# Kernel tuning notes

Hardware: AMD Instinct MI355X
Metric: run time of the kernel (lower is better)

The kernel has to match this reference:

```python
import jax, jax.numpy as jnp
import numpy as np

L_SEQ, BS = 500, 512
STATE, OBS, INP = 64, 64, 32  # estimate_A = eye(obs) acts on state -> state == obs


def setup_inputs() -> dict:
    key = jax.random.key(0)
    ks = jax.random.split(key, 8)
    return {
        "external_input_seq": jax.random.normal(ks[0], (L_SEQ, BS, INP), jnp.float32),
        "observations_seq": jax.random.normal(ks[1], (L_SEQ, BS, OBS), jnp.float32),
        "initial_prior_mu": jax.random.normal(ks[2], (BS, STATE), jnp.float32),
        # sigma must be strictly positive (log is taken); shift uniform away from 0
        "initial_prior_sigma": jax.random.uniform(ks[3], (BS, STATE), jnp.float32) + 0.5,
        # learned params (torch randn init, scaled 0.1 for numerical stability of the recursion)
        "logsigma": jax.random.normal(ks[4], (STATE,), jnp.float32) * 0.1,
        "B": jax.random.normal(ks[5], (STATE, INP), jnp.float32) * 0.1,
        "H": jax.random.normal(ks[6], (OBS, STATE), jnp.float32) * 0.1,
        "logdelta": jax.random.normal(ks[7], (OBS,), jnp.float32) * 0.1,
    }


def reference(external_input_seq, observations_seq, initial_prior_mu,
              initial_prior_sigma, logsigma, B, H, logdelta):
    s = initial_prior_mu.shape[-1]
    dt = initial_prior_mu.dtype
    A = jnp.eye(s, dtype=dt)                    # estimate_A = eye, requires_grad=False
    I = jnp.eye(s, dtype=dt)
    Q = jnp.diag(jnp.exp(logsigma) ** 2)        # process noise cov (s, s)
    Rm = jnp.diag(jnp.exp(logdelta) ** 2)       # observation noise cov (o, o)

    def step(carry, inp):
        mu_prior, cov_prior = carry             # (bs, s), (bs, s, s)
        u_prev, y = inp                         # (bs, inp), (bs, o)
        mu_pred = mu_prior @ A.T + u_prev @ B.T                     # (bs, s)
        cov_pred = A @ cov_prior @ A.T + Q                          # (bs, s, s)
        S = H @ cov_pred @ H.T + Rm                                 # (bs, o, o)
        K = cov_pred @ H.T @ jnp.linalg.inv(S)                      # (bs, s, o)
        innov = y - mu_pred @ H.T                                   # (bs, o)
        mu_post = mu_pred + jnp.einsum('bso,bo->bs', K, innov)      # (bs, s)
        cov_post = (I - K @ H) @ cov_pred                           # (bs, s, s)
        logsig = jnp.log(jnp.sqrt(jnp.diagonal(cov_post, axis1=-2, axis2=-1)))
        return (mu_post, cov_post), (mu_post, logsig)

    cov0 = (initial_prior_sigma ** 2)[..., None] * jnp.eye(s, dtype=dt)  # diag_embed
    _, (mus, logs) = jax.lax.scan(
        step, (initial_prior_mu, cov0),
        (external_input_seq[:-1], observations_seq[1:]))
    state_mu = jnp.concatenate([initial_prior_mu[None], mus], axis=0)          # (l, bs, s)
    state_logsigma = jnp.concatenate([jnp.log(initial_prior_sigma)[None], logs], axis=0)
    return state_mu, state_logsigma
```

## Files before the change

kernel.cpp:

```cpp
#include <hip/hip_runtime.h>
#include <math.h>

#define L_SEQ 500
#define NBS   512
#define N     64
#define NI    32
#define AUGW  132
#define PW    68
#define HW    68

#define OFF_AUG 0
#define OFF_P   (OFF_AUG + 64*AUGW)
#define OFF_H   (OFF_P   + 64*PW)
#define OFF_BT  (OFF_H   + 64*HW)
#define OFF_RK  (OFF_BT  + NI*64)
#define OFF_QD  (OFF_RK  + 64)
#define OFF_RD  (OFF_QD  + 64)
#define OFF_MU  (OFF_RD  + 64)
#define OFF_MUP (OFF_MU  + 64)
#define OFF_WV  (OFF_MUP + 64)
#define OFF_U   (OFF_WV  + 64)
#define OFF_YV  (OFF_U   + 32)
#define OFF_LSC (OFF_YV  + 64)
#define OFF_FLG (OFF_LSC + 64)
#define SM_FLOATS (OFF_FLG + 4)

#define CONV_TAU  2e-5f
#define CONV_MINS 20

union F4 { float4 v; float f[4]; };

#define LW(i,k) Aug[((i)-16)*AUGW + 48 + (k)]

__global__ __launch_bounds__(256, 2)
void akf5(const float* __restrict__ ext,
          const float* __restrict__ obs,
          const float* __restrict__ mu0,
          const float* __restrict__ sg0,
          const float* __restrict__ lsg,
          const float* __restrict__ Bm,
          const float* __restrict__ Hm,
          const float* __restrict__ ldl,
          float* __restrict__ out_mu,
          float* __restrict__ out_ls)
{
    extern __shared__ float sm[];
    float* Aug = sm + OFF_AUG;
    float* P   = sm + OFF_P;
    float* Hs  = sm + OFF_H;
    float* Bt  = sm + OFF_BT;
    float* rk  = sm + OFF_RK;
    float* Qd  = sm + OFF_QD;
    float* Rd  = sm + OFF_RD;
    float* mu  = sm + OFF_MU;
    float* mup = sm + OFF_MUP;
    float* wv  = sm + OFF_WV;
    float* uvec= sm + OFF_U;
    float* yv  = sm + OFF_YV;
    float* lsc = sm + OFF_LSC;
    int*   flagI = (int*)(sm + OFF_FLG);

    const int b   = blockIdx.x;
    const int tid = threadIdx.x;
    const int tx  = tid & 15;
    const int ty  = tid >> 4;

    int Rlow = 0, Clow = 0;
    {
        int t = tid < 136 ? tid : 0;
        int R = (int)((sqrtf(8.0f * (float)t + 1.0f) - 1.0f) * 0.5f);
        if ((R + 1) * (R + 2) / 2 <= t) ++R;
        if (R * (R + 1) / 2 > t) --R;
        Rlow = R; Clow = t - R * (R + 1) / 2;
    }

    if (tid < 64) {
        int i = tid;
        float q = expf(lsg[i]); Qd[i] = q * q;
        float r = expf(ldl[i]); Rd[i] = r * r;
        float m0 = mu0[b * N + i];
        float s0 = sg0[b * N + i];
        mu[i]  = m0;
        mup[i] = s0;
        out_mu[(size_t)b * N + i] = m0;
        out_ls[(size_t)b * N + i] = logf(s0);
        Aug[i * AUGW + 129] = 0.f; Aug[i * AUGW + 130] = 0.f; Aug[i * AUGW + 131] = 0.f;
    }
    if (tid == 0) { flagI[0] = 0; flagI[1] = 0; }
    for (int e = tid; e < N * N; e += 256) {
        Hs[(e >> 6) * HW + (e & 63)] = Hm[e];
    }
    for (int e = tid; e < N * NI; e += 256) {
        int i = e >> 5, k = e & 31;
        Bt[k * 64 + i] = Bm[e];
    }
    __syncthreads();
    for (int e = tid; e < N * N; e += 256) {
        int i = e >> 6, j = e & 63;
        float v = 0.f;
        if (i == j) { float s = mup[i]; v = s * s; }
        P[i * PW + j] = v;
    }
    if (tid >= 192 && tid < 200) {
        int q = tid - 192;
        *(float4*)&uvec[4 * q] = *(const float4*)&ext[(size_t)b * NI + 4 * q];
    }
    if (tid >= 200 && tid < 216) {
        int q = tid - 200;
        *(float4*)&yv[4 * q] = *(const float4*)&obs[(size_t)(NBS + b) * N + 4 * q];
    }
    __syncthreads();

    int streak = 0, sb = 0;

    #pragma unroll 1
    for (int s = 0; s < L_SEQ - 1; ++s) {
        if (tid < 64) {
            float acc = mu[tid];
            #pragma unroll
            for (int k = 0; k < NI; ++k) acc += Bt[k * 64 + tid] * uvec[k];
            mup[tid] = acc;
        }
        __builtin_amdgcn_wave_barrier();
        if (tid < 64) {
            float acc = yv[tid];
            #pragma unroll 4
            for (int c4 = 0; c4 < 16; ++c4) {
                F4 h; h.v = *(const float4*)&Hs[tid * HW + 4 * c4];
                F4 m; m.v = *(const float4*)&mup[4 * c4];
                acc -= h.f[0]*m.f[0] + h.f[1]*m.f[1] + h.f[2]*m.f[2] + h.f[3]*m.f[3];
            }
            Aug[tid * AUGW + 128] = acc;
        }
        {
            const int i0 = 4 * ty, j0 = 4 * tx;
            float acc[4][4];
            F4 qv; qv.v = *(const float4*)&Qd[j0];
            #pragma unroll
            for (int dr = 0; dr < 4; ++dr) {
                F4 hv; hv.v = *(const float4*)&Hs[(i0 + dr) * HW + j0];
                #pragma unroll
                for (int dc = 0; dc < 4; ++dc) acc[dr][dc] = hv.f[dc] * qv.f[dc];
            }
            #pragma unroll 4
            for (int c4 = 0; c4 < 16; ++c4) {
                F4 h4[4], p4[4];
                #pragma unroll
                for (int dr = 0; dr < 4; ++dr) h4[dr].v = *(const float4*)&Hs[(i0 + dr) * HW + 4 * c4];
                #pragma unroll
                for (int dk = 0; dk < 4; ++dk) p4[dk].v = *(const float4*)&P[(4 * c4 + dk) * PW + j0];
                #pragma unroll
                for (int dk = 0; dk < 4; ++dk)
                    #pragma unroll
                    for (int dr = 0; dr < 4; ++dr)
                        #pragma unroll
                        for (int dc = 0; dc < 4; ++dc)
                            acc[dr][dc] += h4[dr].f[dk] * p4[dk].f[dc];
            }
            #pragma unroll
            for (int dr = 0; dr < 4; ++dr) {
                float4 v; v.x = acc[dr][0]; v.y = acc[dr][1]; v.z = acc[dr][2]; v.w = acc[dr][3];
                *(float4*)&Aug[(i0 + dr) * AUGW + 64 + j0] = v;
            }
        }
        __syncthreads();

        if (tid < 136) {
            const int i0 = 4 * Rlow, j0 = 4 * Clow;
            float acc[4][4];
            #pragma unroll
            for (int a = 0; a < 4; ++a)
                #pragma unroll
                for (int c = 0; c < 4; ++c) acc[a][c] = 0.f;
            #pragma unroll 4
            for (int c4 = 0; c4 < 16; ++c4) {
                F4 a4[4], b4[4];
                #pragma unroll
                for (int dr = 0; dr < 4; ++dr) a4[dr].v = *(const float4*)&Aug[(i0 + dr) * AUGW + 64 + 4 * c4];
                #pragma unroll
                for (int dc = 0; dc < 4; ++dc) b4[dc].v = *(const float4*)&Hs[(j0 + dc) * HW + 4 * c4];
                #pragma unroll
                for (int dr = 0; dr < 4; ++dr)
                    #pragma unroll
                    for (int dc = 0; dc < 4; ++dc)
                        #pragma unroll
                        for (int dk = 0; dk < 4; ++dk)
                            acc[dr][dc] += a4[dr].f[dk] * b4[dc].f[dk];
            }
            #pragma unroll
            for (int dr = 0; dr < 4; ++dr) {
                #pragma unroll
                for (int dc = 0; dc < 4; ++dc)
                    if (i0 + dr == j0 + dc) acc[dr][dc] += Rd[i0 + dr];
                float4 v; v.x = acc[dr][0]; v.y = acc[dr][1]; v.z = acc[dr][2]; v.w = acc[dr][3];
                *(float4*)&Aug[(i0 + dr) * AUGW + j0] = v;
            }
        } else if (tid < 200) {
            const int i = tid - 136;
            P[i * PW + i] += Qd[i];
        } else if (tid == 200) {
            flagI[0] = 0; flagI[1] = 0;
        }
        __syncthreads();

        #pragma unroll 1
        for (int p = 0; p < 4; ++p) {
            const int p0 = 16 * p;
            if (tid < 64) {
                const int lane = tid;
                float st[16], lw[16], myrk = 0.f;
                if (lane >= p0) {
                    #pragma unroll
                    for (int q = 0; q < 4; ++q) {
                        F4 t4; t4.v = *(const float4*)&Aug[lane * AUGW + p0 + 4 * q];
                        st[4*q+0] = t4.f[0]; st[4*q+1] = t4.f[1]; st[4*q+2] = t4.f[2]; st[4*q+3] = t4.f[3];
                    }
                } else {
                    #pragma unroll
                    for (int q = 0; q < 16; ++q) st[q] = 0.f;
                }
                #pragma unroll
                for (int kr = 0; kr < 16; ++kr) {
                    const int k = p0 + kr;
                    float dk  = __shfl(st[kr], k, 64);
                    float rkv = 1.0f / dk;
                    if (lane == k) myrk = rkv;
                    float coef = st[kr] * rkv;
                    coef = (lane > k) ? coef : 0.f;
                    lw[kr] = coef;
                    #pragma unroll
                    for (int jr = kr + 1; jr < 16; ++jr) {
                        float wjk = __shfl(st[kr], p0 + jr, 64);
                        st[jr] -= coef * wjk;
                    }
                }
                if (lane >= p0) {
                    #pragma unroll
                    for (int q = 0; q < 4; ++q) {
                        float4 v; v.x = st[4*q+0]; v.y = st[4*q+1]; v.z = st[4*q+2]; v.w = st[4*q+3];
                        *(float4*)&Aug[lane * AUGW + p0 + 4 * q] = v;
                    }
                    if (lane < p0 + 16) rk[lane] = myrk;
                }
                if (lane >= p0 + 16) {
                    #pragma unroll
                    for (int q = 0; q < 4; ++q) {
                        float4 v; v.x = lw[4*q+0]; v.y = lw[4*q+1]; v.z = lw[4*q+2]; v.w = lw[4*q+3];
                        *(float4*)&LW(lane, 4 * q) = v;
                    }
                }
                float ec[16], zr[16];
                #pragma unroll
                for (int r2 = 0; r2 < 16; ++r2) {
                    ec[r2] = Aug[(p0 + r2) * AUGW + 64 + lane];
                    zr[r2] = Aug[(p0 + r2) * AUGW + 128];
                }
                #pragma unroll
                for (int kp = 0; kp < 15; ++kp) {
                    #pragma unroll
                    for (int r2 = kp + 1; r2 < 16; ++r2) {
                        float L = __shfl(lw[kp], p0 + r2, 64);
                        ec[r2] -= L * ec[kp];
                        zr[r2] -= L * zr[kp];
                    }
                }
                #pragma unroll
                for (int r2 = 0; r2 < 16; ++r2)
                    Aug[(p0 + r2) * AUGW + 64 + lane] = ec[r2];
                if (lane == 0) {
                    #pragma unroll
                    for (int r2 = 0; r2 < 16; ++r2)
                        Aug[(p0 + r2) * AUGW + 128] = zr[r2];
                }
            }
            __syncthreads();

            if (p < 3) {
                const int TS  = (p == 0) ? 78 : (p == 1) ? 36 : 10;
                const int rows = 48 - 16 * p;
                const int TE  = (rows / 4) * 17;
                const int tot = TS + TE;
                const int ofs = 4 * (p + 1);
                #pragma unroll 1
                for (int t = tid; t < tot; t += 256) {
                    int i0, Cb; bool isS;
                    if (t < TS) {
                        int rr = (int)((sqrtf(8.0f * (float)t + 1.0f) - 1.0f) * 0.5f);
                        if ((rr + 1) * (rr + 2) / 2 <= t) ++rr;
                        if (rr * (rr + 1) / 2 > t) --rr;
                        int cc = t - rr * (rr + 1) / 2;
                        i0 = 4 * (ofs + rr); Cb = 4 * (ofs + cc); isS = true;
                    } else {
                        int e2 = t - TS;
                        i0 = 4 * (ofs + e2 / 17); Cb = 64 + 4 * (e2 % 17); isS = false;
                    }
                    F4 acc[4];
                    #pragma unroll
                    for (int dr = 0; dr < 4; ++dr) acc[dr].v = *(const float4*)&Aug[(i0 + dr) * AUGW + Cb];
                    #pragma unroll
                    for (int c4 = 0; c4 < 4; ++c4) {
                        F4 a4[4];
                        #pragma unroll
                        for (int dr = 0; dr < 4; ++dr) a4[dr].v = *(const float4*)&LW(i0 + dr, 4 * c4);
                        if (isS) {
                            F4 b4[4];
                            #pragma unroll
                            for (int dc = 0; dc < 4; ++dc) b4[dc].v = *(const float4*)&Aug[(Cb + dc) * AUGW + p0 + 4 * c4];
                            #pragma unroll
                            for (int dr = 0; dr < 4; ++dr)
                                #pragma unroll
                                for (int dc = 0; dc < 4; ++dc)
                                    #pragma unroll
                                    for (int dk = 0; dk < 4; ++dk)
                                        acc[dr].f[dc] -= a4[dr].f[dk] * b4[dc].f[dk];
                        } else {
                            F4 b4[4];
                            #pragma unroll
                            for (int dk = 0; dk < 4; ++dk) b4[dk].v = *(const float4*)&Aug[(p0 + 4 * c4 + dk) * AUGW + Cb];
                            #pragma unroll
                            for (int dk = 0; dk < 4; ++dk)
                                #pragma unroll
                                for (int dr = 0; dr < 4; ++dr)
                                    #pragma unroll
                                    for (int dc = 0; dc < 4; ++dc)
                                        acc[dr].f[dc] -= a4[dr].f[dk] * b4[dk].f[dc];
                        }
                    }
                    #pragma unroll
                    for (int dr = 0; dr < 4; ++dr) *(float4*)&Aug[(i0 + dr) * AUGW + Cb] = acc[dr].v;
                }
                __syncthreads();
            }
        }

        const size_t o = (size_t)((s + 1) * NBS + b) * N;
        float tdmax = 0.f, tpmax = 0.f;
        if (tid < 136) {
            const int i0 = 4 * Rlow, j0 = 4 * Clow;
            F4 acc[4], oldv[4];
            #pragma unroll
            for (int dr = 0; dr < 4; ++dr) { acc[dr].v = *(const float4*)&P[(i0 + dr) * PW + j0]; oldv[dr].v = acc[dr].v; }
            #pragma unroll 2
            for (int c4 = 0; c4 < 16; ++c4) {
                F4 rv; rv.v = *(const float4*)&rk[4 * c4];
                F4 ea[4], eb[4];
                #pragma unroll
                for (int dk = 0; dk < 4; ++dk) ea[dk].v = *(const float4*)&Aug[(4 * c4 + dk) * AUGW + 64 + i0];
                #pragma unroll
                for (int dk = 0; dk < 4; ++dk) eb[dk].v = *(const float4*)&Aug[(4 * c4 + dk) * AUGW + 64 + j0];
                #pragma unroll
                for (int dk = 0; dk < 4; ++dk) {
                    float sc[4];
                    #pragma unroll
                    for (int dr = 0; dr < 4; ++dr) sc[dr] = ea[dk].f[dr] * rv.f[dk];
                    #pragma unroll
                    for (int dr = 0; dr < 4; ++dr)
                        #pragma unroll
                        for (int dc = 0; dc < 4; ++dc)
                            acc[dr].f[dc] -= sc[dr] * eb[dk].f[dc];
                }
            }
            #pragma unroll
            for (int dr = 0; dr < 4; ++dr) *(float4*)&P[(i0 + dr) * PW + j0] = acc[dr].v;
            #pragma unroll
            for (int dr = 0; dr < 4; ++dr)
                #pragma unroll
                for (int dc = 0; dc < 4; ++dc) {
                    float d = acc[dr].f[dc] - oldv[dr].f[dc];
                    if (Rlow == Clow && dr == dc) d += Qd[i0 + dr];
                    tdmax = fmaxf(tdmax, fabsf(d));
                    tpmax = fmaxf(tpmax, fabsf(acc[dr].f[dc]));
                }
            if (Rlow != Clow) {
                #pragma unroll
                for (int dc = 0; dc < 4; ++dc) {
                    float4 v; v.x = acc[0].f[dc]; v.y = acc[1].f[dc]; v.z = acc[2].f[dc]; v.w = acc[3].f[dc];
                    *(float4*)&P[(j0 + dc) * PW + i0] = v;
                }
            } else {
                #pragma unroll
                for (int dr = 0; dr < 4; ++dr)
                    out_ls[o + i0 + dr] = 0.5f * logf(acc[dr].f[dr]);
            }
        }
        if (tid >= 192) {
            const int i = tid - 192;
            wv[i] = rk[i] * Aug[i * AUGW + 128];
            float acc = mup[i];
            #pragma unroll 4
            for (int c4 = 0; c4 < 16; ++c4) {
                F4 wq; wq.v = *(const float4*)&wv[4 * c4];
                #pragma unroll
                for (int dk = 0; dk < 4; ++dk)
                    acc += Aug[(4 * c4 + dk) * AUGW + 64 + i] * wq.f[dk];
            }
            mu[i] = acc;
            out_mu[o + i] = acc;
        }
        if (tid >= 136 && tid < 144) {
            int q = tid - 136;
            *(float4*)&uvec[4 * q] = *(const float4*)&ext[(size_t)((s + 1) * NBS + b) * NI + 4 * q];
        }
        if (tid >= 144 && tid < 160 && s < L_SEQ - 2) {
            int q = tid - 144;
            *(float4*)&yv[4 * q] = *(const float4*)&obs[(size_t)((s + 2) * NBS + b) * N + 4 * q];
        }
        #pragma unroll
        for (int off = 32; off; off >>= 1) {
            tdmax = fmaxf(tdmax, __shfl_xor(tdmax, off, 64));
            tpmax = fmaxf(tpmax, __shfl_xor(tpmax, off, 64));
        }
        if ((tid & 63) == 0) {
            atomicMax(&flagI[0], __float_as_int(tdmax));
            atomicMax(&flagI[1], __float_as_int(tpmax));
        }
        __syncthreads();

        {
            float dm = __int_as_float(flagI[0]);
            float pm = __int_as_float(flagI[1]);
            bool conv = (s >= CONV_MINS) && (dm <= CONV_TAU * pm);
            streak = conv ? (streak + 1) : 0;
            if (streak >= 2) { sb = s + 1; break; }
        }
    }

    if (sb > 0) {
        {
            const int i0 = 4 * ty, j0 = 4 * tx;
            float acc[4][4];
            #pragma unroll
            for (int a = 0; a < 4; ++a)
                #pragma unroll
                for (int c = 0; c < 4; ++c) acc[a][c] = 0.f;
            #pragma unroll 4
            for (int c4 = 0; c4 < 16; ++c4) {
                F4 a4[4], b4[4];
                #pragma unroll
                for (int dr = 0; dr < 4; ++dr) a4[dr].v = *(const float4*)&P[(i0 + dr) * PW + 4 * c4];
                #pragma unroll
                for (int dc = 0; dc < 4; ++dc) b4[dc].v = *(const float4*)&Hs[(j0 + dc) * HW + 4 * c4];
                #pragma unroll
                for (int dr = 0; dr < 4; ++dr)
                    #pragma unroll
                    for (int dc = 0; dc < 4; ++dc)
                        #pragma unroll
                        for (int dk = 0; dk < 4; ++dk)
                            acc[dr][dc] += a4[dr].f[dk] * b4[dc].f[dk];
            }
            float ri[4];
            #pragma unroll
            for (int dc = 0; dc < 4; ++dc) ri[dc] = 1.0f / Rd[j0 + dc];
            #pragma unroll
            for (int dr = 0; dr < 4; ++dr) {
                float4 v; v.x = acc[dr][0]*ri[0]; v.y = acc[dr][1]*ri[1];
                          v.z = acc[dr][2]*ri[2]; v.w = acc[dr][3]*ri[3];
                *(float4*)&Aug[(i0 + dr) * AUGW + 64 + j0] = v;
            }
            if (tid < 64) lsc[tid] = 0.5f * logf(P[tid * PW + tid]);
        }
        __syncthreads();

        #pragma unroll 1
        for (int s2 = sb; s2 < L_SEQ - 1; ++s2) {
            const size_t o2 = (size_t)((s2 + 1) * NBS + b) * N;
            if (tid < 64) {
                float acc = mu[tid];
                #pragma unroll
                for (int k = 0; k < NI; ++k) acc += Bt[k * 64 + tid] * uvec[k];
                mup[tid] = acc;
            }
            __syncthreads();
            if (tid < 64) {
                float acc = yv[tid];
                #pragma unroll 4
                for (int c4 = 0; c4 < 16; ++c4) {
                    F4 h; h.v = *(const float4*)&Hs[tid * HW + 4 * c4];
                    F4 m; m.v = *(const float4*)&mup[4 * c4];
                    acc -= h.f[0]*m.f[0] + h.f[1]*m.f[1] + h.f[2]*m.f[2] + h.f[3]*m.f[3];
                }
                wv[tid] = acc;
                out_ls[o2 + tid] = lsc[tid];
            } else if (tid < 72) {
                int q = tid - 64;
                *(float4*)&uvec[4 * q] = *(const float4*)&ext[(size_t)((s2 + 1) * NBS + b) * NI + 4 * q];
            }
            __syncthreads();
            if (tid < 64) {
                float acc = mup[tid];
                #pragma unroll 4
                for (int c4 = 0; c4 < 16; ++c4) {
                    F4 kg; kg.v = *(const float4*)&Aug[tid * AUGW + 64 + 4 * c4];
                    F4 w;  w.v  = *(const float4*)&wv[4 * c4];
                    acc += kg.f[0]*w.f[0] + kg.f[1]*w.f[1] + kg.f[2]*w.f[2] + kg.f[3]*w.f[3];
                }
                mu[tid] = acc;
                out_mu[o2 + tid] = acc;
            } else if (tid < 80 && s2 < L_SEQ - 2) {
                int q = tid - 64;
                *(float4*)&yv[4 * q] = *(const float4*)&obs[(size_t)((s2 + 2) * NBS + b) * N + 4 * q];
            }
            __syncthreads();
        }
    }
}

extern "C" void kernel_launch(void* const* d_in, const int* in_sizes, int n_in,
                              void* d_out, int out_size, void* d_ws, size_t ws_size,
                              hipStream_t stream) {
    const float* ext = (const float*)d_in[0];
    const float* obs = (const float*)d_in[1];
    const float* mu0 = (const float*)d_in[2];
    const float* sg0 = (const float*)d_in[3];
    const float* lsg = (const float*)d_in[4];
    const float* Bm  = (const float*)d_in[5];
    const float* Hm  = (const float*)d_in[6];
    const float* ldl = (const float*)d_in[7];
    float* out_mu = (float*)d_out;
    float* out_ls = out_mu + (size_t)L_SEQ * NBS * N;

    size_t smem = (size_t)SM_FLOATS * sizeof(float);
    hipFuncSetAttribute(reinterpret_cast<const void*>(akf5),
                        hipFuncAttributeMaxDynamicSharedMemorySize, (int)smem);

    akf5<<<dim3(NBS), dim3(256), smem, stream>>>(
        ext, obs, mu0, sg0, lsg, Bm, Hm, ldl, out_mu, out_ls);
}
```

Before: 14.88 ms.

## Overlap covariance downdate with block LDL factorization and use readlane broadcasts

Moves the rank-update of the covariance into the per-panel loop so warps 1-3 accumulate each finished panel's contribution while warp 0 factorizes the next panel, leaving only the last panel for after the loop. Replaces cross-lane shuffles with readlane scalar broadcasts and the exact reciprocal with the hardware approximate reciprocal. The aim is to shorten the serial critical path per timestep, at the cost of extra registers held across panels and slightly lower reciprocal precision.

```diff
diff --git a/kernel.cpp b/kernel.cpp
--- a/kernel.cpp
+++ b/kernel.cpp
@@ -32,8 +32,12 @@
 
 #define LW(i,k) Aug[((i)-16)*AUGW + 48 + (k)]
 
+__device__ __forceinline__ float rl(float x, int srclane) {
+    return __int_as_float(__builtin_amdgcn_readlane(__float_as_int(x), srclane));
+}
+
 __global__ __launch_bounds__(256, 2)
-void akf5(const float* __restrict__ ext,
+void akf7(const float* __restrict__ ext,
           const float* __restrict__ obs,
           const float* __restrict__ mu0,
           const float* __restrict__ sg0,
@@ -73,6 +77,14 @@
         if (R * (R + 1) / 2 > t) --R;
         Rlow = R; Clow = t - R * (R + 1) / 2;
     }
+    int Rg = 0, Cg = 0;
+    {
+        int t = (tid >= 64 && tid < 200) ? (tid - 64) : 0;
+        int R = (int)((sqrtf(8.0f * (float)t + 1.0f) - 1.0f) * 0.5f);
+        if ((R + 1) * (R + 2) / 2 <= t) ++R;
+        if (R * (R + 1) / 2 > t) --R;
+        Rg = R; Cg = t - R * (R + 1) / 2;
+    }
 
     if (tid < 64) {
         int i = tid;
@@ -203,6 +215,7 @@
         }
         __syncthreads();
 
+        F4 gacc[4];
         #pragma unroll 1
         for (int p = 0; p < 4; ++p) {
             const int p0 = 16 * p;
@@ -222,15 +235,15 @@
                 #pragma unroll
                 for (int kr = 0; kr < 16; ++kr) {
                     const int k = p0 + kr;
-                    float dk  = __shfl(st[kr], k, 64);
-                    float rkv = 1.0f / dk;
+                    float dk  = rl(st[kr], k);
+                    float rkv = __builtin_amdgcn_rcpf(dk);
                     if (lane == k) myrk = rkv;
                     float coef = st[kr] * rkv;
                     coef = (lane > k) ? coef : 0.f;
                     lw[kr] = coef;
                     #pragma unroll
                     for (int jr = kr + 1; jr < 16; ++jr) {
-                        float wjk = __shfl(st[kr], p0 + jr, 64);
+                        float wjk = rl(st[kr], p0 + jr);
                         st[jr] -= coef * wjk;
                     }
                 }
@@ -259,7 +272,7 @@
                 for (int kp = 0; kp < 15; ++kp) {
                     #pragma unroll
                     for (int r2 = kp + 1; r2 < 16; ++r2) {
-                        float L = __shfl(lw[kp], p0 + r2, 64);
+                        float L = rl(lw[kp], p0 + r2);
                         ec[r2] -= L * ec[kp];
                         zr[r2] -= L * zr[kp];
                     }
@@ -271,6 +284,34 @@
                     #pragma unroll
                     for (int r2 = 0; r2 < 16; ++r2)
                         Aug[(p0 + r2) * AUGW + 128] = zr[r2];
+                }
+            } else if (p > 0 && tid < 200) {
+                const int cp = p - 1;
+                const int i0 = 4 * Rg, j0 = 4 * Cg;
+                if (p == 1) {
+                    #pragma unroll
+                    for (int dr = 0; dr < 4; ++dr) gacc[dr].v = *(const float4*)&P[(i0 + dr) * PW + j0];
+                }
+                #pragma unroll
+                for (int q = 0; q < 4; ++q) {
+                    const int c4 = 4 * cp + q;
+                    F4 rv; rv.v = *(const float4*)&rk[4 * c4];
+                    F4 ea[4], eb[4];
+                    #pragma unroll
+                    for (int dk = 0; dk < 4; ++dk) ea[dk].v = *(const float4*)&Aug[(4 * c4 + dk) * AUGW + 64 + i0];
+                    #pragma unroll
+                    for (int dk = 0; dk < 4; ++dk) eb[dk].v = *(const float4*)&Aug[(4 * c4 + dk) * AUGW + 64 + j0];
+                    #pragma unroll
+                    for (int dk = 0; dk < 4; ++dk) {
+                        float sc[4];
+                        #pragma unroll
+                        for (int dr = 0; dr < 4; ++dr) sc[dr] = ea[dk].f[dr] * rv.f[dk];
+                        #pragma unroll
+                        for (int dr = 0; dr < 4; ++dr)
+                            #pragma unroll
+                            for (int dc = 0; dc < 4; ++dc)
+                                gacc[dr].f[dc] -= sc[dr] * eb[dk].f[dc];
+                    }
                 }
             }
             __syncthreads();
@@ -335,13 +376,11 @@
 
         const size_t o = (size_t)((s + 1) * NBS + b) * N;
         float tdmax = 0.f, tpmax = 0.f;
-        if (tid < 136) {
-            const int i0 = 4 * Rlow, j0 = 4 * Clow;
-            F4 acc[4], oldv[4];
-            #pragma unroll
-            for (int dr = 0; dr < 4; ++dr) { acc[dr].v = *(const float4*)&P[(i0 + dr) * PW + j0]; oldv[dr].v = acc[dr].v; }
-            #pragma unroll 2
-            for (int c4 = 0; c4 < 16; ++c4) {
+        if (tid >= 64 && tid < 200) {
+            const int i0 = 4 * Rg, j0 = 4 * Cg;
+            #pragma unroll
+            for (int q = 0; q < 4; ++q) {
+                const int c4 = 12 + q;
                 F4 rv; rv.v = *(const float4*)&rk[4 * c4];
                 F4 ea[4], eb[4];
                 #pragma unroll
@@ -357,34 +396,35 @@
                     for (int dr = 0; dr < 4; ++dr)
                         #pragma unroll
                         for (int dc = 0; dc < 4; ++dc)
-                            acc[dr].f[dc] -= sc[dr] * eb[dk].f[dc];
-                }
-            }
-            #pragma unroll
-            for (int dr = 0; dr < 4; ++dr) *(float4*)&P[(i0 + dr) * PW + j0] = acc[dr].v;
-            #pragma unroll
-            for (int dr = 0; dr < 4; ++dr)
+                            gacc[dr].f[dc] -= sc[dr] * eb[dk].f[dc];
+                }
+            }
+            #pragma unroll
+            for (int dr = 0; dr < 4; ++dr) {
+                F4 oldv; oldv.v = *(const float4*)&P[(i0 + dr) * PW + j0];
                 #pragma unroll
                 for (int dc = 0; dc < 4; ++dc) {
-                    float d = acc[dr].f[dc] - oldv[dr].f[dc];
-                    if (Rlow == Clow && dr == dc) d += Qd[i0 + dr];
+                    float d = gacc[dr].f[dc] - oldv.f[dc];
+                    if (Rg == Cg && dr == dc) d += Qd[i0 + dr];
                     tdmax = fmaxf(tdmax, fabsf(d));
-                    tpmax = fmaxf(tpmax, fabsf(acc[dr].f[dc]));
-                }
-            if (Rlow != Clow) {
+                    tpmax = fmaxf(tpmax, fabsf(gacc[dr].f[dc]));
+                }
+            }
+            #pragma unroll
+            for (int dr = 0; dr < 4; ++dr) *(float4*)&P[(i0 + dr) * PW + j0] = gacc[dr].v;
+            if (Rg != Cg) {
                 #pragma unroll
                 for (int dc = 0; dc < 4; ++dc) {
-                    float4 v; v.x = acc[0].f[dc]; v.y = acc[1].f[dc]; v.z = acc[2].f[dc]; v.w = acc[3].f[dc];
+                    float4 v; v.x = gacc[0].f[dc]; v.y = gacc[1].f[dc]; v.z = gacc[2].f[dc]; v.w = gacc[3].f[dc];
                     *(float4*)&P[(j0 + dc) * PW + i0] = v;
                 }
             } else {
                 #pragma unroll
                 for (int dr = 0; dr < 4; ++dr)
-                    out_ls[o + i0 + dr] = 0.5f * logf(acc[dr].f[dr]);
-            }
-        }
-        if (tid >= 192) {
-            const int i = tid - 192;
+                    out_ls[o + i0 + dr] = 0.5f * logf(gacc[dr].f[dr]);
+            }
+        } else if (tid < 64) {
+            const int i = tid;
             wv[i] = rk[i] * Aug[i * AUGW + 128];
             float acc = mup[i];
             #pragma unroll 4
@@ -397,12 +437,12 @@
             mu[i] = acc;
             out_mu[o + i] = acc;
         }
-        if (tid >= 136 && tid < 144) {
-            int q = tid - 136;
+        if (tid >= 200 && tid < 208) {
+            int q = tid - 200;
             *(float4*)&uvec[4 * q] = *(const float4*)&ext[(size_t)((s + 1) * NBS + b) * NI + 4 * q];
         }
-        if (tid >= 144 && tid < 160 && s < L_SEQ - 2) {
-            int q = tid - 144;
+        if (tid >= 208 && tid < 224 && s < L_SEQ - 2) {
+            int q = tid - 208;
             *(float4*)&yv[4 * q] = *(const float4*)&obs[(size_t)((s + 2) * NBS + b) * N + 4 * q];
         }
         #pragma unroll
@@ -520,9 +560,9 @@
     float* out_ls = out_mu + (size_t)L_SEQ * NBS * N;
 
     size_t smem = (size_t)SM_FLOATS * sizeof(float);
-    hipFuncSetAttribute(reinterpret_cast<const void*>(akf5),
+    hipFuncSetAttribute(reinterpret_cast<const void*>(akf7),
                         hipFuncAttributeMaxDynamicSharedMemorySize, (int)smem);
 
-    akf5<<<dim3(NBS), dim3(256), smem, stream>>>(
+    akf7<<<dim3(NBS), dim3(256), smem, stream>>>(
         ext, obs, mu0, sg0, lsg, Bm, Hm, ldl, out_mu, out_ls);
 }
```

Measured after the change: 13.62 ms. 8.4% less time.
